# Kernel tuning notes

Hardware: AMD Instinct MI355X
Metric: run time of the kernel (lower is better)

Reference implementation:

```python
import jax, jax.numpy as jnp
import numpy as np

H = 16
D_MODEL = 1024
D_K = D_MODEL // H
SEQ = 2048
BATCH = 2


def setup_inputs() -> dict:
    key = jax.random.key(0)
    ks = jax.random.split(key, 11)
    s = 1.0 / np.sqrt(D_MODEL)
    inp = {
        "query": jax.random.normal(ks[0], (SEQ, BATCH, D_MODEL), jnp.float32),
        "key_": jax.random.normal(ks[1], (SEQ, BATCH, D_MODEL), jnp.float32),
        "value": jax.random.normal(ks[2], (SEQ, BATCH, D_MODEL), jnp.float32),
        "Wq": jax.random.uniform(ks[3], (D_MODEL, D_MODEL), jnp.float32, -s, s),
        "bq": jax.random.uniform(ks[4], (D_MODEL,), jnp.float32, -s, s),
        "Wk": jax.random.uniform(ks[5], (D_MODEL, D_MODEL), jnp.float32, -s, s),
        "bk": jax.random.uniform(ks[6], (D_MODEL,), jnp.float32, -s, s),
        "Wv": jax.random.uniform(ks[7], (D_MODEL, D_MODEL), jnp.float32, -s, s),
        "bv": jax.random.uniform(ks[8], (D_MODEL,), jnp.float32, -s, s),
        "Wo": jax.random.uniform(ks[9], (D_MODEL, D_MODEL), jnp.float32, -s, s),
        "bo": jax.random.uniform(ks[10], (D_MODEL,), jnp.float32, -s, s),
    }
    return inp


def _mha(query, key_, value, Wq, bq, Wk, bk, Wv, bv, Wo, bo):
    S, B, D = query.shape
    # torch Linear: x @ W.T + b; then view(S,B,h,dk).transpose(0,2) -> [h,B,S,dk]
    def proj(x, W, b):
        return jnp.transpose((x @ W.T + b).reshape(S, B, H, D_K), (2, 1, 0, 3))

    q = proj(query, Wq, bq)   # [h, b, S, dk]
    k = proj(key_, Wk, bk)
    v = proj(value, Wv, bv)

    scores = jnp.einsum("hbqd,hbkd->hbqk", q, k) / jnp.sqrt(
        jnp.asarray(D_K, q.dtype)
    )  # [h, b, S, S]
    p_attn = jax.nn.softmax(scores, axis=-1)  # dropout p=0.0 -> identity
    x = jnp.einsum("hbqk,hbkd->hbqd", p_attn, v)  # [h, b, S, dk]
    x = jnp.transpose(x, (2, 1, 0, 3)).reshape(S, B, D)  # back to [S, B, D]
    return x @ Wo.T + bo


def reference(query, key_, value, Wq, bq, Wk, bk, Wv, bv, Wo, bo):
    return _mha(query, key_, value, Wq, bq, Wk, bk, Wv, bv, Wo, bo)
```

## Files before the change

### kernel.cpp

```cpp
#include <hip/hip_runtime.h>

#define SEQ   2048
#define BATCH 2
#define DM    1024
#define NH    16
#define DKD   64
#define MROWS (SEQ*BATCH)

#define QSCALE 0.18033688011112042f

using bf16x8 = __attribute__((ext_vector_type(8))) __bf16;
using bf16x4 = __attribute__((ext_vector_type(4))) __bf16;
using bf16x2 = __attribute__((ext_vector_type(2))) __bf16;
using f32x4  = __attribute__((ext_vector_type(4))) float;

__device__ __forceinline__ void gld_lds16(const __bf16* g, __bf16* l) {
  __builtin_amdgcn_global_load_lds(
      (__attribute__((address_space(1))) void*)(g),
      (__attribute__((address_space(3))) void*)(l), 16, 0, 0);
}

__global__ __launch_bounds__(256) void cvt_all(
    const float* __restrict__ s0, const float* __restrict__ s1,
    const float* __restrict__ s2, const float* __restrict__ s3,
    const float* __restrict__ s4, const float* __restrict__ s5,
    const float* __restrict__ s6,
    __bf16* __restrict__ d0, __bf16* __restrict__ d1, __bf16* __restrict__ d2,
    __bf16* __restrict__ d3, __bf16* __restrict__ d4, __bf16* __restrict__ d5,
    __bf16* __restrict__ d6, int n_big, int n_small) {
  int y = blockIdx.y;
  const float* s; __bf16* d;
  switch (y) {
    case 0: s = s0; d = d0; break;
    case 1: s = s1; d = d1; break;
    case 2: s = s2; d = d2; break;
    case 3: s = s3; d = d3; break;
    case 4: s = s4; d = d4; break;
    case 5: s = s5; d = d5; break;
    default: s = s6; d = d6; break;
  }
  int n = (y < 3) ? n_big : n_small;
  int i = (blockIdx.x * 256 + threadIdx.x) * 8;
  if (i >= n) return;
  const float4* sp = (const float4*)(s + i);
  float4 a = sp[0], b = sp[1];
  bf16x8 v;
  v[0]=(__bf16)a.x; v[1]=(__bf16)a.y; v[2]=(__bf16)a.z; v[3]=(__bf16)a.w;
  v[4]=(__bf16)b.x; v[5]=(__bf16)b.y; v[6]=(__bf16)b.z; v[7]=(__bf16)b.w;
  *(bf16x8*)(d + i) = v;
}

__device__ __forceinline__ void gemm_core(const __bf16* __restrict__ A,
                                          const __bf16* __restrict__ Bt,
                                          __bf16* Ash, __bf16* Bsh,
                                          f32x4 acc[4][4], int m0, int n0) {
  const int K = DM;
  int tid = threadIdx.x;
  int lane = tid & 63, quad = lane >> 4, l16 = lane & 15;
  int w = tid >> 6;
  int wm = (w & 1) * 64, wn = (w >> 1) * 64;
  for (int k0 = 0; k0 < K; k0 += 32) {
    __syncthreads();
#pragma unroll
    for (int it = 0; it < 2; ++it) {
      int c   = tid + it * 256;
      int row = c >> 2, ko = (c & 3) * 8;
      int base = (tid - lane + it * 256) * 8;
      gld_lds16(A  + (size_t)(m0 + row) * K + k0 + ko, Ash + base);
      gld_lds16(Bt + (size_t)(n0 + row) * K + k0 + ko, Bsh + base);
    }
    __syncthreads();
    bf16x8 af[4], bfr[4];
#pragma unroll
    for (int mi = 0; mi < 4; mi++)
      af[mi] = *(const bf16x8*)&Ash[(wm + mi * 16 + l16) * 32 + quad * 8];
#pragma unroll
    for (int ni = 0; ni < 4; ni++)
      bfr[ni] = *(const bf16x8*)&Bsh[(wn + ni * 16 + l16) * 32 + quad * 8];
#pragma unroll
    for (int mi = 0; mi < 4; mi++)
#pragma unroll
      for (int ni = 0; ni < 4; ni++)
        acc[mi][ni] = __builtin_amdgcn_mfma_f32_16x16x32_bf16(
            af[mi], bfr[ni], acc[mi][ni], 0, 0, 0);
  }
}

__global__ __launch_bounds__(256, 3) void gemm_qkv(
    const __bf16* __restrict__ Xq, const __bf16* __restrict__ Xk,
    const __bf16* __restrict__ Xv, const __bf16* __restrict__ Wqkv,
    const float* __restrict__ bqp, const float* __restrict__ bkp,
    const float* __restrict__ bvp,
    __bf16* __restrict__ Qb, __bf16* __restrict__ Kb, __bf16* __restrict__ Vt) {
  __shared__ __bf16 Ash[128 * 32], Bsh[128 * 32];
  __shared__ __bf16 Esh[4][16 * 72];
  int z = blockIdx.z;
  const __bf16* A   = (z == 0) ? Xq : (z == 1) ? Xk : Xv;
  const __bf16* Bt  = Wqkv + (size_t)z * (DM * DM);
  const float* bias = (z == 0) ? bqp : (z == 1) ? bkp : bvp;
  int m0 = blockIdx.y * 128, n0 = blockIdx.x * 128;
  f32x4 acc[4][4] = {};
  gemm_core(A, Bt, Ash, Bsh, acc, m0, n0);

  int tid = threadIdx.x, lane = tid & 63, quad = lane >> 4, l16 = lane & 15;
  int w = tid >> 6, wm = (w & 1) * 64, wn = (w >> 1) * 64;
  __bf16* E = Esh[w];
  int n_base = n0 + wn;
  int hh = n_base >> 6;
  float scale = (z == 0) ? QSCALE : 1.0f;
  float bb[4];
#pragma unroll
  for (int ni = 0; ni < 4; ni++) bb[ni] = bias[n_base + ni * 16 + l16] * scale;

  if (z == 2) {
#pragma unroll
    for (int ni = 0; ni < 4; ni++) {
#pragma unroll
      for (int mi = 0; mi < 4; mi++) {
        int s0 = mi * 8 + quad * 2;
        bf16x2 p0, p1;
        p0[0] = (__bf16)(acc[mi][ni][0] + bb[ni]);
        p0[1] = (__bf16)(acc[mi][ni][2] + bb[ni]);
        p1[0] = (__bf16)(acc[mi][ni][1] + bb[ni]);
        p1[1] = (__bf16)(acc[mi][ni][3] + bb[ni]);
        *(bf16x2*)&E[l16 * 72 + s0]      = p0;
        *(bf16x2*)&E[l16 * 72 + 32 + s0] = p1;
      }
      asm volatile("s_waitcnt lgkmcnt(0)" ::: "memory");
#pragma unroll
      for (int pass = 0; pass < 2; pass++) {
        int ddl = pass * 8 + (lane >> 3);
        int col = (lane & 7) * 8;
        bf16x8 v = *(const bf16x8*)&E[ddl * 72 + col];
        int b2 = col >> 5, sl = col & 31;
        int dd = ni * 16 + ddl;
        int sg = ((m0 + wm) >> 1) + sl;
        *(bf16x8*)&Vt[(((size_t)hh * BATCH + b2) * DKD + dd) * SEQ + sg] = v;
      }
      asm volatile("s_waitcnt lgkmcnt(0)" ::: "memory");
    }
  } else {
    __bf16* Out = (z == 0) ? Qb : Kb;
#pragma unroll
    for (int mi = 0; mi < 4; mi++) {
#pragma unroll
      for (int ni = 0; ni < 4; ni++)
#pragma unroll
        for (int r = 0; r < 4; r++)
          E[(quad * 4 + r) * 72 + ni * 16 + l16] =
              (__bf16)fmaf(acc[mi][ni][r], scale, bb[ni]);
      asm volatile("s_waitcnt lgkmcnt(0)" ::: "memory");
#pragma unroll
      for (int pass = 0; pass < 2; pass++) {
        int row16 = pass * 8 + (lane >> 3);
        int coll  = (lane & 7) * 8;
        bf16x8 v = *(const bf16x8*)&E[row16 * 72 + coll];
        int m = m0 + wm + mi * 16 + row16;
        int s = m >> 1, b2 = m & 1;
        *(bf16x8*)&Out[(((size_t)hh * BATCH + b2) * SEQ + s) * DKD + coll] = v;
      }
      asm volatile("s_waitcnt lgkmcnt(0)" ::: "memory");
    }
  }
}

__global__ __launch_bounds__(256, 3) void gemm_out(
    const __bf16* __restrict__ A, const __bf16* __restrict__ Bt,
    const float* __restrict__ bias, float* __restrict__ out) {
  __shared__ __bf16 Ash[64 * 32], Bsh[128 * 32];
  const int K = DM;
  int m0 = blockIdx.y * 64, n0 = blockIdx.x * 128;
  int tid = threadIdx.x;
  int lane = tid & 63, quad = lane >> 4, l16 = lane & 15;
  int w = tid >> 6;
  int wm = (w & 1) * 32, wn = (w >> 1) * 64;
  f32x4 acc[2][4] = {};
  for (int k0 = 0; k0 < K; k0 += 32) {
    __syncthreads();
    {
      int c = tid;
      int row = c >> 2, ko = (c & 3) * 8;
      gld_lds16(A + (size_t)(m0 + row) * K + k0 + ko,
                Ash + (tid - lane) * 8);
    }
#pragma unroll
    for (int it = 0; it < 2; ++it) {
      int c = tid + it * 256;
      int row = c >> 2, ko = (c & 3) * 8;
      gld_lds16(Bt + (size_t)(n0 + row) * K + k0 + ko,
                Bsh + (tid - lane + it * 256) * 8);
    }
    __syncthreads();
    bf16x8 af[2], bfr[4];
#pragma unroll
    for (int mi = 0; mi < 2; mi++)
      af[mi] = *(const bf16x8*)&Ash[(wm + mi * 16 + l16) * 32 + quad * 8];
#pragma unroll
    for (int ni = 0; ni < 4; ni++)
      bfr[ni] = *(const bf16x8*)&Bsh[(wn + ni * 16 + l16) * 32 + quad * 8];
#pragma unroll
    for (int mi = 0; mi < 2; mi++)
#pragma unroll
      for (int ni = 0; ni < 4; ni++)
        acc[mi][ni] = __builtin_amdgcn_mfma_f32_16x16x32_bf16(
            af[mi], bfr[ni], acc[mi][ni], 0, 0, 0);
  }
#pragma unroll
  for (int ni = 0; ni < 4; ni++) {
    int n = n0 + wn + ni * 16 + l16;
    float bb = bias[n];
#pragma unroll
    for (int mi = 0; mi < 2; mi++) {
#pragma unroll
      for (int r = 0; r < 4; r++) {
        int m = m0 + wm + mi * 16 + quad * 4 + r;
        out[(size_t)m * DM + n] = acc[mi][ni][r] + bb;
      }
    }
  }
}

__global__ __launch_bounds__(256, 2) void flash_attn(
    const __bf16* __restrict__ Qg, const __bf16* __restrict__ Kg,
    const __bf16* __restrict__ Vtg, __bf16* __restrict__ Xa) {
  __shared__ __bf16 Ksh[2][64 * 64];
  __shared__ __bf16 Vsh[2][64 * 64];
  __shared__ __bf16 Psh[4][32 * 64];
  int tid = threadIdx.x, w = tid >> 6, lane = tid & 63;
  int quad = lane >> 4, l16 = lane & 15, sw = l16 & 7;
  int h = blockIdx.z, b = blockIdx.y, q0 = blockIdx.x * 128;
  size_t hb = ((size_t)h * BATCH + b) * SEQ * DKD;
  const __bf16* Qp = Qg + hb;
  const __bf16* Kp = Kg + hb;
  const __bf16* Vp = Vtg + hb;
  __bf16* Pw = Psh[w];

  bf16x8 qf[2][2];
#pragma unroll
  for (int qb = 0; qb < 2; qb++)
#pragma unroll
    for (int kk = 0; kk < 2; kk++)
      qf[qb][kk] = *(const bf16x8*)(
          Qp + (size_t)(q0 + w * 32 + qb * 16 + l16) * DKD + kk * 32 + quad * 8);

  f32x4 o[2][4] = {};
  float l_[2] = {0.f, 0.f};

#pragma unroll
  for (int it = 0; it < 2; ++it) {
    int c = tid + it * 256;
    int r = c >> 3, pp = c & 7;
    int off = (pp ^ (r & 7)) << 3;
    gld_lds16(Kp + (size_t)r * DKD + off, Ksh[0] + c * 8);
    gld_lds16(Vp + (size_t)r * SEQ + off, Vsh[0] + c * 8);
  }

  for (int t = 0; t < SEQ / 64; ++t) {
    __syncthreads();
    if (t + 1 < SEQ / 64) {
      int k0n = (t + 1) * 64, bn = (t + 1) & 1;
#pragma unroll
      for (int it = 0; it < 2; ++it) {
        int c = tid + it * 256;
        int r = c >> 3, pp = c & 7;
        int off = (pp ^ (r & 7)) << 3;
        gld_lds16(Kp + (size_t)(k0n + r) * DKD + off, Ksh[bn] + c * 8);
        gld_lds16(Vp + (size_t)r * SEQ + k0n + off, Vsh[bn] + c * 8);
      }
    }
    const __bf16* Kb_ = Ksh[t & 1];
    const __bf16* Vb_ = Vsh[t & 1];

    f32x4 sc[2][4];
#pragma unroll
    for (int ji = 0; ji < 4; ji++) {
      int rr = ji * 16 + l16;
      bf16x8 kf0 = *(const bf16x8*)&Kb_[rr * 64 + ((quad ^ sw) << 3)];
      bf16x8 kf1 = *(const bf16x8*)&Kb_[rr * 64 + (((4 + quad) ^ sw) << 3)];
#pragma unroll
      for (int qb = 0; qb < 2; qb++) {
        f32x4 t2 = {0.f, 0.f, 0.f, 0.f};
        t2 = __builtin_amdgcn_mfma_f32_16x16x32_bf16(kf0, qf[qb][0], t2, 0, 0, 0);
        t2 = __builtin_amdgcn_mfma_f32_16x16x32_bf16(kf1, qf[qb][1], t2, 0, 0, 0);
        sc[qb][ji] = t2;
      }
    }

#pragma unroll
    for (int qb = 0; qb < 2; qb++) {
#pragma unroll
      for (int ji = 0; ji < 4; ji++) {
        bf16x4 pk;
#pragma unroll
        for (int r = 0; r < 4; r++) {
          float pv = exp2f(sc[qb][ji][r]);
          l_[qb] += pv;
          pk[r] = (__bf16)pv;
        }
        *(bf16x4*)&Pw[(qb * 16 + l16) * 64 +
                      (((ji * 2 + (quad >> 1)) ^ sw) << 3) + ((quad & 1) << 2)] = pk;
      }
    }

#pragma unroll
    for (int kk = 0; kk < 2; kk++) {
      bf16x8 pa[2];
#pragma unroll
      for (int qb = 0; qb < 2; qb++)
        pa[qb] = *(const bf16x8*)&Pw[(qb * 16 + l16) * 64 +
                                     (((kk * 4 + quad) ^ sw) << 3)];
#pragma unroll
      for (int ni = 0; ni < 4; ni++) {
        int rr = ni * 16 + l16;
        bf16x8 vb = *(const bf16x8*)&Vb_[rr * 64 + (((kk * 4 + quad) ^ sw) << 3)];
#pragma unroll
        for (int qb = 0; qb < 2; qb++)
          o[qb][ni] = __builtin_amdgcn_mfma_f32_16x16x32_bf16(pa[qb], vb,
                                                              o[qb][ni], 0, 0, 0);
      }
    }
  }

#pragma unroll
  for (int qb = 0; qb < 2; qb++) {
    l_[qb] += __shfl_xor(l_[qb], 16, 64);
    l_[qb] += __shfl_xor(l_[qb], 32, 64);
    l_[qb] = 1.0f / l_[qb];
  }
#pragma unroll
  for (int qb = 0; qb < 2; qb++)
#pragma unroll
    for (int r = 0; r < 4; r++) {
      float li = __shfl(l_[qb], quad * 4 + r, 64);
      int q = q0 + w * 32 + qb * 16 + quad * 4 + r;
#pragma unroll
      for (int ni = 0; ni < 4; ni++) {
        int d = ni * 16 + l16;
        Xa[((size_t)q * BATCH + b) * DM + h * DKD + d] =
            (__bf16)(o[qb][ni][r] * li);
      }
    }
}

extern "C" void kernel_launch(void* const* d_in, const int* in_sizes, int n_in,
                              void* d_out, int out_size, void* d_ws,
                              size_t ws_size, hipStream_t stream) {
  (void)in_sizes; (void)n_in; (void)out_size; (void)ws_size;
  const float* query = (const float*)d_in[0];
  const float* key_  = (const float*)d_in[1];
  const float* value = (const float*)d_in[2];
  const float* Wq = (const float*)d_in[3];
  const float* bq = (const float*)d_in[4];
  const float* Wk = (const float*)d_in[5];
  const float* bk = (const float*)d_in[6];
  const float* Wv = (const float*)d_in[7];
  const float* bv = (const float*)d_in[8];
  const float* Wo = (const float*)d_in[9];
  const float* bo = (const float*)d_in[10];

  const size_t NX = (size_t)MROWS * DM;
  const size_t NW = (size_t)DM * DM;
  __bf16* p    = (__bf16*)d_ws;
  __bf16* Xq   = p; p += NX;
  __bf16* Xk   = p; p += NX;
  __bf16* Xv   = p; p += NX;
  __bf16* Wqkv = p; p += 3 * NW;
  __bf16* Wob  = p; p += NW;
  __bf16* Qb   = p; p += NX;
  __bf16* Kb   = p; p += NX;
  __bf16* Vt   = p; p += NX;
  __bf16* Xa   = p; p += NX;

  cvt_all<<<dim3((unsigned)(NX / 2048), 7), 256, 0, stream>>>(
      query, key_, value, Wq, Wk, Wv, Wo,
      Xq, Xk, Xv, Wqkv, Wqkv + NW, Wqkv + 2 * NW, Wob, (int)NX, (int)NW);

  gemm_qkv<<<dim3(DM / 128, MROWS / 128, 3), 256, 0, stream>>>(
      Xq, Xk, Xv, Wqkv, bq, bk, bv, Qb, Kb, Vt);
  flash_attn<<<dim3(SEQ / 128, BATCH, NH), 256, 0, stream>>>(Qb, Kb, Vt, Xa);
  gemm_out<<<dim3(DM / 128, MROWS / 64), 256, 0, stream>>>(
      Xa, Wob, bo, (float*)d_out);
}
```

Before: 240.7 us.

## Shrink flash-attention blocks to 64 queries and single-buffer K/V tiles

The attention kernel now uses 128-thread blocks that each handle 64 queries. It launches a flat 1024-block grid with head/batch as the fast-varying index. K/V tiles go into a single LDS buffer that is loaded synchronously each step, with a second barrier before use. The intent is to raise block count and occupancy and cut LDS use. In exchange, the double-buffered prefetch overlap is gone and each K/V tile is reused by half as many queries, doubling global K/V traffic.

```diff
diff --git a/kernel.cpp b/kernel.cpp
--- a/kernel.cpp
+++ b/kernel.cpp
@@ -220,19 +220,21 @@
   }
 }
 
-__global__ __launch_bounds__(256, 2) void flash_attn(
+__global__ __launch_bounds__(128, 2) void flash_attn(
     const __bf16* __restrict__ Qg, const __bf16* __restrict__ Kg,
     const __bf16* __restrict__ Vtg, __bf16* __restrict__ Xa) {
-  __shared__ __bf16 Ksh[2][64 * 64];
-  __shared__ __bf16 Vsh[2][64 * 64];
-  __shared__ __bf16 Psh[4][32 * 64];
+  __shared__ __bf16 Ksh[64 * 64];
+  __shared__ __bf16 Vsh[64 * 64];
+  __shared__ __bf16 Psh[2][32 * 64];
   int tid = threadIdx.x, w = tid >> 6, lane = tid & 63;
   int quad = lane >> 4, l16 = lane & 15, sw = l16 & 7;
-  int h = blockIdx.z, b = blockIdx.y, q0 = blockIdx.x * 128;
-  size_t hb = ((size_t)h * BATCH + b) * SEQ * DKD;
-  const __bf16* Qp = Qg + hb;
-  const __bf16* Kp = Kg + hb;
-  const __bf16* Vp = Vtg + hb;
+  int n = blockIdx.x;
+  int hb = n & 31, qi = n >> 5;
+  int h = hb >> 1, b = hb & 1, q0 = qi * 64;
+  size_t hboff = ((size_t)h * BATCH + b) * SEQ * DKD;
+  const __bf16* Qp = Qg + hboff;
+  const __bf16* Kp = Kg + hboff;
+  const __bf16* Vp = Vtg + hboff;
   __bf16* Pw = Psh[w];
 
   bf16x8 qf[2][2];
@@ -246,37 +248,31 @@
   f32x4 o[2][4] = {};
   float l_[2] = {0.f, 0.f};
 
-#pragma unroll
-  for (int it = 0; it < 2; ++it) {
-    int c = tid + it * 256;
-    int r = c >> 3, pp = c & 7;
-    int off = (pp ^ (r & 7)) << 3;
-    gld_lds16(Kp + (size_t)r * DKD + off, Ksh[0] + c * 8);
-    gld_lds16(Vp + (size_t)r * SEQ + off, Vsh[0] + c * 8);
-  }
-
   for (int t = 0; t < SEQ / 64; ++t) {
-    __syncthreads();
-    if (t + 1 < SEQ / 64) {
-      int k0n = (t + 1) * 64, bn = (t + 1) & 1;
-#pragma unroll
-      for (int it = 0; it < 2; ++it) {
-        int c = tid + it * 256;
-        int r = c >> 3, pp = c & 7;
-        int off = (pp ^ (r & 7)) << 3;
-        gld_lds16(Kp + (size_t)(k0n + r) * DKD + off, Ksh[bn] + c * 8);
-        gld_lds16(Vp + (size_t)r * SEQ + k0n + off, Vsh[bn] + c * 8);
-      }
-    }
-    const __bf16* Kb_ = Ksh[t & 1];
-    const __bf16* Vb_ = Vsh[t & 1];
+    int k0 = t * 64;
+    __syncthreads();
+#pragma unroll
+    for (int it = 0; it < 4; ++it) {
+      int c = tid + it * 128;
+      int r = c >> 3, pp = c & 7;
+      int off = (pp ^ (r & 7)) << 3;
+      gld_lds16(Kp + (size_t)(k0 + r) * DKD + off, Ksh + c * 8);
+    }
+#pragma unroll
+    for (int it = 0; it < 4; ++it) {
+      int c = tid + it * 128;
+      int r = c >> 3, pp = c & 7;
+      int off = (pp ^ (r & 7)) << 3;
+      gld_lds16(Vp + (size_t)r * SEQ + k0 + off, Vsh + c * 8);
+    }
+    __syncthreads();
 
     f32x4 sc[2][4];
 #pragma unroll
     for (int ji = 0; ji < 4; ji++) {
       int rr = ji * 16 + l16;
-      bf16x8 kf0 = *(const bf16x8*)&Kb_[rr * 64 + ((quad ^ sw) << 3)];
-      bf16x8 kf1 = *(const bf16x8*)&Kb_[rr * 64 + (((4 + quad) ^ sw) << 3)];
+      bf16x8 kf0 = *(const bf16x8*)&Ksh[rr * 64 + ((quad ^ sw) << 3)];
+      bf16x8 kf1 = *(const bf16x8*)&Ksh[rr * 64 + (((4 + quad) ^ sw) << 3)];
 #pragma unroll
       for (int qb = 0; qb < 2; qb++) {
         f32x4 t2 = {0.f, 0.f, 0.f, 0.f};
@@ -312,7 +308,7 @@
 #pragma unroll
       for (int ni = 0; ni < 4; ni++) {
         int rr = ni * 16 + l16;
-        bf16x8 vb = *(const bf16x8*)&Vb_[rr * 64 + (((kk * 4 + quad) ^ sw) << 3)];
+        bf16x8 vb = *(const bf16x8*)&Vsh[rr * 64 + (((kk * 4 + quad) ^ sw) << 3)];
 #pragma unroll
         for (int qb = 0; qb < 2; qb++)
           o[qb][ni] = __builtin_amdgcn_mfma_f32_16x16x32_bf16(pa[qb], vb,
@@ -377,7 +373,7 @@
 
   gemm_qkv<<<dim3(DM / 128, MROWS / 128, 3), 256, 0, stream>>>(
       Xq, Xk, Xv, Wqkv, bq, bk, bv, Qb, Kb, Vt);
-  flash_attn<<<dim3(SEQ / 128, BATCH, NH), 256, 0, stream>>>(Qb, Kb, Vt, Xa);
+  flash_attn<<<dim3(1024), 128, 0, stream>>>(Qb, Kb, Vt, Xa);
   gemm_out<<<dim3(DM / 128, MROWS / 64), 256, 0, stream>>>(
       Xa, Wob, bo, (float*)d_out);
 }
```

After: 247.1 us. 2.6% more time.
